# Kernel tuning notes

Hardware: AMD Instinct MI355X
Metric: run time of the kernel (lower is better)

## Reference

```python
import jax, jax.numpy as jnp
import numpy as np

N_PAPER = 200000
N_MESH = 30000
N = N_PAPER + N_MESH
D_PAPER = 512
D_MESH = 128
E_TRAIN = 2000000
E_POS = 500000
E_NEG = 500000


def setup_inputs() -> dict:
    key = jax.random.key(0)
    ks = jax.random.split(key, 32)

    def w(k, shape, fan_in):
        return jax.random.normal(k, shape, jnp.float32) / np.float32(np.sqrt(fan_in))

    inp = {}
    inp['x_paper'] = jax.random.normal(ks[0], (N_PAPER, D_PAPER), jnp.float32)
    inp['x_mesh'] = jax.random.normal(ks[1], (N_MESH, D_MESH), jnp.float32)
    # input transforms (stored as [in, out]; y = x @ W + b)
    inp['tp_w'] = w(ks[2], (D_PAPER, 16), D_PAPER)
    inp['tp_b'] = jnp.zeros((16,), jnp.float32)
    inp['tm_w'] = w(ks[3], (D_MESH, 16), D_MESH)
    inp['tm_b'] = jnp.zeros((16,), jnp.float32)
    # RGCN layers: basis decomposition W_r = sum_b comp[r,b] * basis[b]
    inp['comp1'] = w(ks[4], (2, 4), 4)
    inp['basis1'] = w(ks[5], (4, 16, 32), 16)
    inp['root1'] = w(ks[6], (16, 32), 16)
    inp['bias1'] = jnp.zeros((32,), jnp.float32)
    inp['comp2'] = w(ks[7], (2, 4), 4)
    inp['basis2'] = w(ks[8], (4, 32, 32), 32)
    inp['root2'] = w(ks[9], (32, 32), 32)
    inp['bias2'] = jnp.zeros((32,), jnp.float32)
    inp['comp3'] = w(ks[10], (2, 4), 4)
    inp['basis3'] = w(ks[11], (4, 32, 16), 32)
    inp['root3'] = w(ks[12], (32, 16), 32)
    inp['bias3'] = jnp.zeros((16,), jnp.float32)
    # decode linears (16 -> 16)
    inp['dpp_w'] = w(ks[13], (16, 16), 16)
    inp['dpp_b'] = jnp.zeros((16,), jnp.float32)
    inp['dpm_w'] = w(ks[14], (16, 16), 16)
    inp['dpm_b'] = jnp.zeros((16,), jnp.float32)
    # graph structure
    inp['train_edge_index'] = jax.random.randint(ks[15], (2, E_TRAIN), 0, N, jnp.int64)
    inp['train_edge_type'] = jax.random.randint(ks[16], (E_TRAIN,), 0, 2, jnp.int64)
    inp['pos_edge_index'] = jax.random.randint(ks[17], (2, E_POS), 0, N, jnp.int64)
    inp['pos_edge_type'] = jnp.sort(jax.random.randint(ks[18], (E_POS,), 0, 2, jnp.int64))
    inp['neg_edge_index'] = jax.random.randint(ks[19], (2, E_NEG), 0, N, jnp.int64)
    inp['neg_edge_type'] = jnp.sort(jax.random.randint(ks[20], (E_NEG,), 0, 2, jnp.int64))
    return inp


def rgcn(x, src, dst, etype, comp, basis, root, bias):
    # W: [R, in, out] from basis decomposition
    W = jnp.einsum('rb,bio->rio', comp, basis)
    # relation-typed message per edge (R == 2: compute both, select)
    xs = x[src]                                   # [E, in]  gather
    m = jnp.where((etype == 0)[:, None], xs @ W[0], xs @ W[1])  # [E, out]
    n = x.shape[0]
    agg = jax.ops.segment_sum(m, dst, num_segments=n)           # scatter-add
    deg = jax.ops.segment_sum(jnp.ones((src.shape[0],), x.dtype), dst, num_segments=n)
    agg = agg / jnp.maximum(deg, 1.0)[:, None]                   # mean aggregation
    return agg + x @ root + bias


def reference(x_paper, x_mesh, tp_w, tp_b, tm_w, tm_b,
              comp1, basis1, root1, bias1,
              comp2, basis2, root2, bias2,
              comp3, basis3, root3, bias3,
              dpp_w, dpp_b, dpm_w, dpm_b,
              train_edge_index, train_edge_type,
              pos_edge_index, pos_edge_type,
              neg_edge_index, neg_edge_type):
    # encode
    x = jnp.concatenate([x_paper @ tp_w + tp_b, x_mesh @ tm_w + tm_b], axis=0)
    src, dst = train_edge_index[0], train_edge_index[1]
    x = jax.nn.relu(rgcn(x, src, dst, train_edge_type, comp1, basis1, root1, bias1))
    x = jax.nn.relu(rgcn(x, src, dst, train_edge_type, comp2, basis2, root2, bias2))
    z = rgcn(x, src, dst, train_edge_type, comp3, basis3, root3, bias3)

    # decode: edge types are sorted, so per-edge type-select equals the
    # original mask-then-concat ordering [type0 ..., type1 ...]
    def edge_scores(ei, et):
        zs, zd = z[ei[0]], z[ei[1]]
        p = jnp.where((et == 0)[:, None], zs @ dpp_w + dpp_b, zs @ dpm_w + dpm_b)
        return (p * zd).sum(-1)

    return jnp.concatenate([edge_scores(pos_edge_index, pos_edge_type),
                            edge_scores(neg_edge_index, neg_edge_type)], axis=0)
```

## Files before the change

### kernel.cpp

```cpp
#include <hip/hip_runtime.h>

#define NPAPER 200000
#define NMESH  30000
#define NNODES 230000
#define ETRAIN 2000000
#define EPOS   500000
#define ENEG   500000

typedef _Float16 f16;
typedef __attribute__((ext_vector_type(8))) _Float16 f16x8;
typedef __attribute__((ext_vector_type(4))) _Float16 f16x4;

__device__ __forceinline__ void fma4(float4& a, float s, const float4 w) {
    a.x = fmaf(s, w.x, a.x);
    a.y = fmaf(s, w.y, a.y);
    a.z = fmaf(s, w.z, a.z);
    a.w = fmaf(s, w.w, a.w);
}

template <int D>
__global__ __launch_bounds__(256) void encode_kernel(
    const float* __restrict__ x, const float* __restrict__ w,
    const float* __restrict__ bias, float* __restrict__ out, int nrows) {
    constexpr int KP = 16;
    __shared__ float wlds[D * 16];
    __shared__ float xlds[256 * 20];
    __shared__ float blds[16];

    for (int i = threadIdx.x; i < D * 4; i += 256)
        reinterpret_cast<float4*>(wlds)[i] =
            reinterpret_cast<const float4*>(w)[i];
    if (threadIdx.x < 16) blds[threadIdx.x] = bias[threadIdx.x];

    const int g = threadIdx.x & 3;
    const int rg = threadIdx.x >> 2;
    const int row0 = blockIdx.x * 256;

    float4 acc[4];
#pragma unroll
    for (int j = 0; j < 4; j++) acc[j] = make_float4(0.f, 0.f, 0.f, 0.f);

    for (int p = 0; p < D / KP; p++) {
        __syncthreads();
        for (int i = threadIdx.x; i < 1024; i += 256) {
            const int rr = i >> 2, q = i & 3;
            const int grow = min(row0 + rr, nrows - 1);
            *reinterpret_cast<float4*>(xlds + rr * 20 + q * 4) =
                *reinterpret_cast<const float4*>(x + (size_t)grow * D +
                                                 p * KP + q * 4);
        }
        __syncthreads();
#pragma unroll
        for (int q = 0; q < KP / 4; q++) {
            const int k = p * KP + q * 4;
            const float4 w0 =
                *reinterpret_cast<const float4*>(wlds + (k + 0) * 16 + 4 * g);
            const float4 w1 =
                *reinterpret_cast<const float4*>(wlds + (k + 1) * 16 + 4 * g);
            const float4 w2 =
                *reinterpret_cast<const float4*>(wlds + (k + 2) * 16 + 4 * g);
            const float4 w3 =
                *reinterpret_cast<const float4*>(wlds + (k + 3) * 16 + 4 * g);
#pragma unroll
            for (int j = 0; j < 4; j++) {
                const float4 xv = *reinterpret_cast<const float4*>(
                    xlds + (rg + 64 * j) * 20 + q * 4);
                fma4(acc[j], xv.x, w0);
                fma4(acc[j], xv.y, w1);
                fma4(acc[j], xv.z, w2);
                fma4(acc[j], xv.w, w3);
            }
        }
    }

    const float4 b4 = *reinterpret_cast<const float4*>(blds + 4 * g);
#pragma unroll
    for (int j = 0; j < 4; j++) {
        const int grow = row0 + rg + 64 * j;
        if (grow < nrows) {
            float4 o;
            o.x = acc[j].x + b4.x;
            o.y = acc[j].y + b4.y;
            o.z = acc[j].z + b4.z;
            o.w = acc[j].w + b4.w;
            *reinterpret_cast<float4*>(out + (size_t)grow * 16 + 4 * g) = o;
        }
    }
}

__global__ __launch_bounds__(256) void hist_kernel(const int* __restrict__ dst,
                                                   int* __restrict__ cnt) {
    const int e = blockIdx.x * 256 + threadIdx.x;
    if (e >= ETRAIN) return;
    atomicAdd(cnt + dst[e], 1);
}

__global__ __launch_bounds__(256) void scan1_kernel(const int* __restrict__ in,
                                                    int* __restrict__ out,
                                                    int* __restrict__ bsum,
                                                    int n) {
    __shared__ int s[256];
    const int tid = threadIdx.x;
    const int i = blockIdx.x * 256 + tid;
    const int v = (i < n) ? in[i] : 0;
    s[tid] = v;
    __syncthreads();
#pragma unroll
    for (int off = 1; off < 256; off <<= 1) {
        const int t = (tid >= off) ? s[tid - off] : 0;
        __syncthreads();
        s[tid] += t;
        __syncthreads();
    }
    if (i < n) out[i] = s[tid] - v;
    if (tid == 255) bsum[blockIdx.x] = s[255];
}

__global__ __launch_bounds__(256) void scan2_kernel(int* __restrict__ bsum,
                                                    int nb) {
    __shared__ int s[256];
    const int tid = threadIdx.x;
    int carry = 0;
    for (int base = 0; base < nb; base += 256) {
        const int i = base + tid;
        const int v = (i < nb) ? bsum[i] : 0;
        s[tid] = v;
        __syncthreads();
#pragma unroll
        for (int off = 1; off < 256; off <<= 1) {
            const int t = (tid >= off) ? s[tid - off] : 0;
            __syncthreads();
            s[tid] += t;
            __syncthreads();
        }
        if (i < nb) bsum[i] = s[tid] - v + carry;
        const int tot = s[255];
        __syncthreads();
        carry += tot;
    }
}

__global__ __launch_bounds__(256) void fill_kernel(
    const int* __restrict__ src, const int* __restrict__ dst,
    const int* __restrict__ et, const int* __restrict__ rowptr,
    const int* __restrict__ bsum, int* __restrict__ fc,
    int* __restrict__ esorted) {
    const int e = blockIdx.x * 256 + threadIdx.x;
    if (e >= ETRAIN) return;
    const int d = dst[e];
    const int pos = rowptr[d] + bsum[d >> 8] + atomicAdd(fc + d, 1);
    esorted[pos] = src[e] | (et[e] << 24);
}

template <int IN, int OUT, bool INH>
__global__ __launch_bounds__(256) void transform_kernel(
    const void* __restrict__ xinp, const float* __restrict__ comp,
    const float* __restrict__ basis, const float* __restrict__ root,
    const float* __restrict__ bias, f16* __restrict__ tcat,
    float* __restrict__ rbuf) {
    constexpr int QP = OUT / 4;
    __shared__ float wl[3 * IN * OUT];
    __shared__ float bl[OUT];
    for (int i = threadIdx.x; i < 2 * IN * OUT; i += 256) {
        const int rr = i / (IN * OUT);
        const int rem = i - rr * IN * OUT;
        float v = 0.f;
#pragma unroll
        for (int bb = 0; bb < 4; bb++)
            v = fmaf(comp[rr * 4 + bb], basis[bb * IN * OUT + rem], v);
        wl[i] = v;
    }
    for (int i = threadIdx.x; i < IN * OUT; i += 256)
        wl[2 * IN * OUT + i] = root[i];
    if (threadIdx.x < OUT) bl[threadIdx.x] = bias[threadIdx.x];
    __syncthreads();

    const int gtid = blockIdx.x * 256 + threadIdx.x;
    const int n = gtid / QP;
    const int g = gtid % QP;
    if (n >= NNODES) return;

    float4 a0 = make_float4(0.f, 0.f, 0.f, 0.f);
    float4 a1 = a0;
    float4 ar = *reinterpret_cast<const float4*>(bl + 4 * g);

    if constexpr (INH) {
        const f16* xin = (const f16*)xinp + (size_t)n * IN;
#pragma unroll
        for (int q = 0; q < IN / 8; q++) {
            const f16x8 raw = reinterpret_cast<const f16x8*>(xin)[q];
#pragma unroll
            for (int j = 0; j < 8; j++) {
                const float xv = (float)raw[j];
                const float* w0 = wl + (q * 8 + j) * OUT + 4 * g;
                fma4(a0, xv, *reinterpret_cast<const float4*>(w0));
                fma4(a1, xv, *reinterpret_cast<const float4*>(w0 + IN * OUT));
                fma4(ar, xv,
                     *reinterpret_cast<const float4*>(w0 + 2 * IN * OUT));
            }
        }
    } else {
        const float* xin = (const float*)xinp + (size_t)n * IN;
#pragma unroll
        for (int q = 0; q < IN / 4; q++) {
            const float4 xv4 = reinterpret_cast<const float4*>(xin)[q];
            const float xs[4] = {xv4.x, xv4.y, xv4.z, xv4.w};
#pragma unroll
            for (int j = 0; j < 4; j++) {
                const float* w0 = wl + (q * 4 + j) * OUT + 4 * g;
                fma4(a0, xs[j], *reinterpret_cast<const float4*>(w0));
                fma4(a1, xs[j],
                     *reinterpret_cast<const float4*>(w0 + IN * OUT));
                fma4(ar, xs[j],
                     *reinterpret_cast<const float4*>(w0 + 2 * IN * OUT));
            }
        }
    }
    f16x4 t0, t1;
    t0[0] = (f16)a0.x; t0[1] = (f16)a0.y; t0[2] = (f16)a0.z; t0[3] = (f16)a0.w;
    t1[0] = (f16)a1.x; t1[1] = (f16)a1.y; t1[2] = (f16)a1.z; t1[3] = (f16)a1.w;
    f16* trow = tcat + (size_t)n * 2 * OUT;
    reinterpret_cast<f16x4*>(trow)[g] = t0;
    reinterpret_cast<f16x4*>(trow + OUT)[g] = t1;
    reinterpret_cast<float4*>(rbuf + (size_t)n * OUT)[g] = ar;
}

template <int OUT, bool RELU, bool OUTH>
__global__ __launch_bounds__(256) void aggroot_kernel(
    const f16* __restrict__ tcat, const float* __restrict__ rbuf,
    const int* __restrict__ rowptr, const int* __restrict__ bsum,
    const int* __restrict__ cnt, const int* __restrict__ esorted,
    void* __restrict__ outp) {
    constexpr int NF = OUT / 4;
    const int gtid = blockIdx.x * 256 + threadIdx.x;
    const int n = gtid >> 5;
    if (n >= NNODES) return;
    const int lane = gtid & 31;
    const int f = lane & 3;
    const int e = lane >> 2;
    const int b = rowptr[n] + bsum[n >> 8];
    const int c = cnt[n];

    float a[NF];
#pragma unroll
    for (int j = 0; j < NF; j++) a[j] = 0.f;

    int i = e;
    int pk = (i < c) ? esorted[b + i] : 0;
    while (i < c) {
        const int in2 = i + 8;
        const int pkn = (in2 < c) ? esorted[b + in2] : 0;
        const int s = pk & 0x00FFFFFF;
        const int t = pk >> 24;
        const f16* row = tcat + ((size_t)s * 2 + t) * OUT + f * NF;
        if constexpr (NF == 8) {
            const f16x8 raw = *reinterpret_cast<const f16x8*>(row);
#pragma unroll
            for (int j = 0; j < 8; j++) a[j] += (float)raw[j];
        } else {
            const f16x4 raw = *reinterpret_cast<const f16x4*>(row);
#pragma unroll
            for (int j = 0; j < 4; j++) a[j] += (float)raw[j];
        }
        pk = pkn;
        i = in2;
    }
#pragma unroll
    for (int m = 4; m <= 16; m <<= 1) {
#pragma unroll
        for (int j = 0; j < NF; j++) a[j] += __shfl_xor(a[j], m);
    }
    const float inv = 1.0f / fmaxf((float)c, 1.0f);
    if constexpr (NF == 8) {
        if (e < 2) {
            const int off = f * 8 + e * 4;
            const float4 rv =
                *reinterpret_cast<const float4*>(rbuf + (size_t)n * OUT + off);
            float4 v;
            v.x = fmaf(a[e * 4 + 0], inv, rv.x);
            v.y = fmaf(a[e * 4 + 1], inv, rv.y);
            v.z = fmaf(a[e * 4 + 2], inv, rv.z);
            v.w = fmaf(a[e * 4 + 3], inv, rv.w);
            if (RELU) {
                v.x = fmaxf(v.x, 0.f);
                v.y = fmaxf(v.y, 0.f);
                v.z = fmaxf(v.z, 0.f);
                v.w = fmaxf(v.w, 0.f);
            }
            if constexpr (OUTH) {
                f16x4 hv;
                hv[0] = (f16)v.x; hv[1] = (f16)v.y;
                hv[2] = (f16)v.z; hv[3] = (f16)v.w;
                *reinterpret_cast<f16x4*>((f16*)outp + (size_t)n * OUT + off) =
                    hv;
            } else {
                *reinterpret_cast<float4*>((float*)outp + (size_t)n * OUT +
                                           off) = v;
            }
        }
    } else {
        if (e == 0) {
            const int off = f * 4;
            const float4 rv =
                *reinterpret_cast<const float4*>(rbuf + (size_t)n * OUT + off);
            float4 v;
            v.x = fmaf(a[0], inv, rv.x);
            v.y = fmaf(a[1], inv, rv.y);
            v.z = fmaf(a[2], inv, rv.z);
            v.w = fmaf(a[3], inv, rv.w);
            if (RELU) {
                v.x = fmaxf(v.x, 0.f);
                v.y = fmaxf(v.y, 0.f);
                v.z = fmaxf(v.z, 0.f);
                v.w = fmaxf(v.w, 0.f);
            }
            if constexpr (OUTH) {
                f16x4 hv;
                hv[0] = (f16)v.x; hv[1] = (f16)v.y;
                hv[2] = (f16)v.z; hv[3] = (f16)v.w;
                *reinterpret_cast<f16x4*>((f16*)outp + (size_t)n * OUT + off) =
                    hv;
            } else {
                *reinterpret_cast<float4*>((float*)outp + (size_t)n * OUT +
                                           off) = v;
            }
        }
    }
}

__global__ __launch_bounds__(256) void decode_kernel(
    const float* __restrict__ z, const int* __restrict__ pei,
    const int* __restrict__ pet, const int* __restrict__ nei,
    const int* __restrict__ net, const float* __restrict__ wp,
    const float* __restrict__ bp, const float* __restrict__ wm,
    const float* __restrict__ bm, float* __restrict__ out) {
    __shared__ float wl[2 * 256];
    __shared__ float bl[2 * 16];
    {
        const int i = threadIdx.x;
        wl[i] = wp[i];
        wl[256 + i] = wm[i];
        if (i < 16) {
            bl[i] = bp[i];
            bl[16 + i] = bm[i];
        }
    }
    __syncthreads();

    const int gtid = blockIdx.x * 256 + threadIdx.x;
    const int e = gtid >> 2;
    const int f = gtid & 3;
    if (e >= EPOS + ENEG) return;
    int s, d, t;
    if (e < EPOS) {
        s = pei[e];
        d = pei[e + EPOS];
        t = pet[e];
    } else {
        const int ee = e - EPOS;
        s = nei[ee];
        d = nei[ee + ENEG];
        t = net[ee];
    }

    const float4 zs = reinterpret_cast<const float4*>(z + (size_t)s * 16)[f];
    const float4 zd = reinterpret_cast<const float4*>(z + (size_t)d * 16)[f];

    const float* W = wl + t * 256;
    float4 p[4];
    if (f == 0) {
#pragma unroll
        for (int g = 0; g < 4; g++)
            p[g] = reinterpret_cast<const float4*>(bl + t * 16)[g];
    } else {
#pragma unroll
        for (int g = 0; g < 4; g++) p[g] = make_float4(0.f, 0.f, 0.f, 0.f);
    }
    const float xs[4] = {zs.x, zs.y, zs.z, zs.w};
#pragma unroll
    for (int c = 0; c < 4; c++) {
        const float4* wr =
            reinterpret_cast<const float4*>(W + (4 * f + c) * 16);
#pragma unroll
        for (int g = 0; g < 4; g++) fma4(p[g], xs[c], wr[g]);
    }
    float* pp = reinterpret_cast<float*>(p);
#pragma unroll
    for (int m = 1; m <= 2; m <<= 1) {
#pragma unroll
        for (int j = 0; j < 16; j++) pp[j] += __shfl_xor(pp[j], m);
    }
    float4 pf;
    if (f == 0) pf = p[0];
    else if (f == 1) pf = p[1];
    else if (f == 2) pf = p[2];
    else pf = p[3];
    float sc = pf.x * zd.x + pf.y * zd.y + pf.z * zd.z + pf.w * zd.w;
    sc += __shfl_xor(sc, 1);
    sc += __shfl_xor(sc, 2);
    if (f == 0) out[e] = sc;
}

extern "C" void kernel_launch(void* const* d_in, const int* in_sizes, int n_in,
                              void* d_out, int out_size, void* d_ws,
                              size_t ws_size, hipStream_t stream) {
    const float* x_paper = (const float*)d_in[0];
    const float* x_mesh = (const float*)d_in[1];
    const float* tp_w = (const float*)d_in[2];
    const float* tp_b = (const float*)d_in[3];
    const float* tm_w = (const float*)d_in[4];
    const float* tm_b = (const float*)d_in[5];
    const float* comp1 = (const float*)d_in[6];
    const float* basis1 = (const float*)d_in[7];
    const float* root1 = (const float*)d_in[8];
    const float* bias1 = (const float*)d_in[9];
    const float* comp2 = (const float*)d_in[10];
    const float* basis2 = (const float*)d_in[11];
    const float* root2 = (const float*)d_in[12];
    const float* bias2 = (const float*)d_in[13];
    const float* comp3 = (const float*)d_in[14];
    const float* basis3 = (const float*)d_in[15];
    const float* root3 = (const float*)d_in[16];
    const float* bias3 = (const float*)d_in[17];
    const float* dpp_w = (const float*)d_in[18];
    const float* dpp_b = (const float*)d_in[19];
    const float* dpm_w = (const float*)d_in[20];
    const float* dpm_b = (const float*)d_in[21];
    const int* tei = (const int*)d_in[22];
    const int* tet = (const int*)d_in[23];
    const int* pei = (const int*)d_in[24];
    const int* pet = (const int*)d_in[25];
    const int* nei = (const int*)d_in[26];
    const int* net = (const int*)d_in[27];
    float* out = (float*)d_out;

    const size_t N = NNODES;
    float* ws = (float*)d_ws;
    float* xfeat = ws;
    float* z = ws + 16 * N;
    float* rbuf = ws + 32 * N;
    f16* tcat = (f16*)(ws + 64 * N);
    f16* h1 = (f16*)(ws + 96 * N);
    f16* h2 = (f16*)(ws + 112 * N);
    int* rowptr = (int*)(ws + 128 * N);
    int* ecnt = rowptr + N;
    int* fc = ecnt + N;
    int* esorted = fc + N;
    int* bsum = esorted + ETRAIN;

    const int* tsrc = tei;
    const int* tdst = tei + ETRAIN;

    const int eblocks = (ETRAIN + 255) / 256;
    const int nb = (NNODES + 255) / 256;
    const int aggb = (NNODES * 32 + 255) / 256;

    encode_kernel<512><<<(NPAPER + 255) / 256, 256, 0, stream>>>(
        x_paper, tp_w, tp_b, xfeat, NPAPER);
    encode_kernel<128><<<(NMESH + 255) / 256, 256, 0, stream>>>(
        x_mesh, tm_w, tm_b, xfeat + (size_t)NPAPER * 16, NMESH);

    hipMemsetAsync(ecnt, 0, (size_t)2 * NNODES * 4, stream);
    hist_kernel<<<eblocks, 256, 0, stream>>>(tdst, ecnt);
    scan1_kernel<<<nb, 256, 0, stream>>>(ecnt, rowptr, bsum, NNODES);
    scan2_kernel<<<1, 256, 0, stream>>>(bsum, nb);
    fill_kernel<<<eblocks, 256, 0, stream>>>(tsrc, tdst, tet, rowptr, bsum,
                                             fc, esorted);

    transform_kernel<16, 32, false>
        <<<(NNODES * 8 + 255) / 256, 256, 0, stream>>>(xfeat, comp1, basis1,
                                                       root1, bias1, tcat,
                                                       rbuf);
    aggroot_kernel<32, true, true><<<aggb, 256, 0, stream>>>(
        tcat, rbuf, rowptr, bsum, ecnt, esorted, h1);

    transform_kernel<32, 32, true>
        <<<(NNODES * 8 + 255) / 256, 256, 0, stream>>>(h1, comp2, basis2,
                                                       root2, bias2, tcat,
                                                       rbuf);
    aggroot_kernel<32, true, true><<<aggb, 256, 0, stream>>>(
        tcat, rbuf, rowptr, bsum, ecnt, esorted, h2);

    transform_kernel<32, 16, true>
        <<<(NNODES * 4 + 255) / 256, 256, 0, stream>>>(h2, comp3, basis3,
                                                       root3, bias3, tcat,
                                                       rbuf);
    aggroot_kernel<16, false, false><<<aggb, 256, 0, stream>>>(
        tcat, rbuf, rowptr, bsum, ecnt, esorted, z);

    decode_kernel<<<((EPOS + ENEG) * 4 + 255) / 256, 256, 0, stream>>>(
        z, pei, pet, nei, net, dpp_w, dpp_b, dpm_w, dpm_b, out);
}
```

Measured before the change: 1.152 ms.

## Precompute per-node decode projections and store root/z buffers in fp16

Decoding now projects every node through both decode linears once (uproj_kernel) instead of recomputing the 16x16 projection per edge, so each edge does only a 16-wide dot product against precomputed fp16 rows. The root-transform buffer and the final embedding z are stored in fp16, halving their memory traffic. Per-node projection adds work over 230k nodes for both types while removing per-edge matmuls on 1M edges, and the extra fp16 rounding adds precision risk.

```diff
diff --git a/kernel.cpp b/kernel.cpp
--- a/kernel.cpp
+++ b/kernel.cpp
@@ -157,7 +157,7 @@
     const void* __restrict__ xinp, const float* __restrict__ comp,
     const float* __restrict__ basis, const float* __restrict__ root,
     const float* __restrict__ bias, f16* __restrict__ tcat,
-    float* __restrict__ rbuf) {
+    f16* __restrict__ rbuf) {
     constexpr int QP = OUT / 4;
     __shared__ float wl[3 * IN * OUT];
     __shared__ float bl[OUT];
@@ -216,18 +216,19 @@
             }
         }
     }
-    f16x4 t0, t1;
+    f16x4 t0, t1, tr;
     t0[0] = (f16)a0.x; t0[1] = (f16)a0.y; t0[2] = (f16)a0.z; t0[3] = (f16)a0.w;
     t1[0] = (f16)a1.x; t1[1] = (f16)a1.y; t1[2] = (f16)a1.z; t1[3] = (f16)a1.w;
+    tr[0] = (f16)ar.x; tr[1] = (f16)ar.y; tr[2] = (f16)ar.z; tr[3] = (f16)ar.w;
     f16* trow = tcat + (size_t)n * 2 * OUT;
     reinterpret_cast<f16x4*>(trow)[g] = t0;
     reinterpret_cast<f16x4*>(trow + OUT)[g] = t1;
-    reinterpret_cast<float4*>(rbuf + (size_t)n * OUT)[g] = ar;
+    reinterpret_cast<f16x4*>(rbuf + (size_t)n * OUT)[g] = tr;
 }
 
 template <int OUT, bool RELU, bool OUTH>
 __global__ __launch_bounds__(256) void aggroot_kernel(
-    const f16* __restrict__ tcat, const float* __restrict__ rbuf,
+    const f16* __restrict__ tcat, const f16* __restrict__ rbuf,
     const int* __restrict__ rowptr, const int* __restrict__ bsum,
     const int* __restrict__ cnt, const int* __restrict__ esorted,
     void* __restrict__ outp) {
@@ -274,13 +275,13 @@
     if constexpr (NF == 8) {
         if (e < 2) {
             const int off = f * 8 + e * 4;
-            const float4 rv =
-                *reinterpret_cast<const float4*>(rbuf + (size_t)n * OUT + off);
+            const f16x4 rv =
+                *reinterpret_cast<const f16x4*>(rbuf + (size_t)n * OUT + off);
             float4 v;
-            v.x = fmaf(a[e * 4 + 0], inv, rv.x);
-            v.y = fmaf(a[e * 4 + 1], inv, rv.y);
-            v.z = fmaf(a[e * 4 + 2], inv, rv.z);
-            v.w = fmaf(a[e * 4 + 3], inv, rv.w);
+            v.x = fmaf(a[e * 4 + 0], inv, (float)rv[0]);
+            v.y = fmaf(a[e * 4 + 1], inv, (float)rv[1]);
+            v.z = fmaf(a[e * 4 + 2], inv, (float)rv[2]);
+            v.w = fmaf(a[e * 4 + 3], inv, (float)rv[3]);
             if (RELU) {
                 v.x = fmaxf(v.x, 0.f);
                 v.y = fmaxf(v.y, 0.f);
@@ -301,13 +302,13 @@
     } else {
         if (e == 0) {
             const int off = f * 4;
-            const float4 rv =
-                *reinterpret_cast<const float4*>(rbuf + (size_t)n * OUT + off);
+            const f16x4 rv =
+                *reinterpret_cast<const f16x4*>(rbuf + (size_t)n * OUT + off);
             float4 v;
-            v.x = fmaf(a[0], inv, rv.x);
-            v.y = fmaf(a[1], inv, rv.y);
-            v.z = fmaf(a[2], inv, rv.z);
-            v.w = fmaf(a[3], inv, rv.w);
+            v.x = fmaf(a[0], inv, (float)rv[0]);
+            v.y = fmaf(a[1], inv, (float)rv[1]);
+            v.z = fmaf(a[2], inv, (float)rv[2]);
+            v.w = fmaf(a[3], inv, (float)rv[3]);
             if (RELU) {
                 v.x = fmaxf(v.x, 0.f);
                 v.y = fmaxf(v.y, 0.f);
@@ -328,12 +329,10 @@
     }
 }
 
-__global__ __launch_bounds__(256) void decode_kernel(
-    const float* __restrict__ z, const int* __restrict__ pei,
-    const int* __restrict__ pet, const int* __restrict__ nei,
-    const int* __restrict__ net, const float* __restrict__ wp,
+__global__ __launch_bounds__(256) void uproj_kernel(
+    const f16* __restrict__ zh, const float* __restrict__ wp,
     const float* __restrict__ bp, const float* __restrict__ wm,
-    const float* __restrict__ bm, float* __restrict__ out) {
+    const float* __restrict__ bm, f16* __restrict__ u) {
     __shared__ float wl[2 * 256];
     __shared__ float bl[2 * 16];
     {
@@ -346,10 +345,48 @@
         }
     }
     __syncthreads();
-
     const int gtid = blockIdx.x * 256 + threadIdx.x;
-    const int e = gtid >> 2;
-    const int f = gtid & 3;
+    const int n = gtid >> 1;
+    const int t = gtid & 1;
+    if (n >= NNODES) return;
+    const f16x8 z0 = reinterpret_cast<const f16x8*>(zh + (size_t)n * 16)[0];
+    const f16x8 z1 = reinterpret_cast<const f16x8*>(zh + (size_t)n * 16)[1];
+    float acc[16];
+#pragma unroll
+    for (int j = 0; j < 16; j++) acc[j] = bl[t * 16 + j];
+    const float* W = wl + t * 256;
+#pragma unroll
+    for (int k = 0; k < 8; k++) {
+        const float zk = (float)z0[k];
+#pragma unroll
+        for (int j = 0; j < 16; j++) acc[j] = fmaf(zk, W[k * 16 + j], acc[j]);
+    }
+#pragma unroll
+    for (int k = 0; k < 8; k++) {
+        const float zk = (float)z1[k];
+#pragma unroll
+        for (int j = 0; j < 16; j++)
+            acc[j] = fmaf(zk, W[(8 + k) * 16 + j], acc[j]);
+    }
+    f16x8 o0, o1;
+#pragma unroll
+    for (int j = 0; j < 8; j++) {
+        o0[j] = (f16)acc[j];
+        o1[j] = (f16)acc[8 + j];
+    }
+    f16* ur = u + (size_t)n * 32 + t * 16;
+    reinterpret_cast<f16x8*>(ur)[0] = o0;
+    reinterpret_cast<f16x8*>(ur)[1] = o1;
+}
+
+__global__ __launch_bounds__(256) void decode_kernel(
+    const f16* __restrict__ u, const f16* __restrict__ zh,
+    const int* __restrict__ pei, const int* __restrict__ pet,
+    const int* __restrict__ nei, const int* __restrict__ net,
+    float* __restrict__ out) {
+    const int gtid = blockIdx.x * 256 + threadIdx.x;
+    const int e = gtid >> 1;
+    const int h = gtid & 1;
     if (e >= EPOS + ENEG) return;
     int s, d, t;
     if (e < EPOS) {
@@ -362,43 +399,15 @@
         d = nei[ee + ENEG];
         t = net[ee];
     }
-
-    const float4 zs = reinterpret_cast<const float4*>(z + (size_t)s * 16)[f];
-    const float4 zd = reinterpret_cast<const float4*>(z + (size_t)d * 16)[f];
-
-    const float* W = wl + t * 256;
-    float4 p[4];
-    if (f == 0) {
-#pragma unroll
-        for (int g = 0; g < 4; g++)
-            p[g] = reinterpret_cast<const float4*>(bl + t * 16)[g];
-    } else {
-#pragma unroll
-        for (int g = 0; g < 4; g++) p[g] = make_float4(0.f, 0.f, 0.f, 0.f);
-    }
-    const float xs[4] = {zs.x, zs.y, zs.z, zs.w};
-#pragma unroll
-    for (int c = 0; c < 4; c++) {
-        const float4* wr =
-            reinterpret_cast<const float4*>(W + (4 * f + c) * 16);
-#pragma unroll
-        for (int g = 0; g < 4; g++) fma4(p[g], xs[c], wr[g]);
-    }
-    float* pp = reinterpret_cast<float*>(p);
-#pragma unroll
-    for (int m = 1; m <= 2; m <<= 1) {
-#pragma unroll
-        for (int j = 0; j < 16; j++) pp[j] += __shfl_xor(pp[j], m);
-    }
-    float4 pf;
-    if (f == 0) pf = p[0];
-    else if (f == 1) pf = p[1];
-    else if (f == 2) pf = p[2];
-    else pf = p[3];
-    float sc = pf.x * zd.x + pf.y * zd.y + pf.z * zd.z + pf.w * zd.w;
+    const f16x8 uv =
+        *reinterpret_cast<const f16x8*>(u + (size_t)s * 32 + t * 16 + h * 8);
+    const f16x8 zv =
+        *reinterpret_cast<const f16x8*>(zh + (size_t)d * 16 + h * 8);
+    float sc = 0.f;
+#pragma unroll
+    for (int j = 0; j < 8; j++) sc = fmaf((float)uv[j], (float)zv[j], sc);
     sc += __shfl_xor(sc, 1);
-    sc += __shfl_xor(sc, 2);
-    if (f == 0) out[e] = sc;
+    if (h == 0) out[e] = sc;
 }
 
 extern "C" void kernel_launch(void* const* d_in, const int* in_sizes, int n_in,
@@ -437,12 +446,13 @@
     const size_t N = NNODES;
     float* ws = (float*)d_ws;
     float* xfeat = ws;
-    float* z = ws + 16 * N;
-    float* rbuf = ws + 32 * N;
-    f16* tcat = (f16*)(ws + 64 * N);
-    f16* h1 = (f16*)(ws + 96 * N);
-    f16* h2 = (f16*)(ws + 112 * N);
-    int* rowptr = (int*)(ws + 128 * N);
+    f16* rbuf = (f16*)(ws + 16 * N);
+    f16* tcat = (f16*)(ws + 32 * N);
+    f16* h1 = (f16*)(ws + 64 * N);
+    f16* h2 = (f16*)(ws + 80 * N);
+    f16* zh = (f16*)(ws + 96 * N);
+    f16* u = (f16*)(ws + 104 * N);
+    int* rowptr = (int*)(ws + 120 * N);
     int* ecnt = rowptr + N;
     int* fc = ecnt + N;
     int* esorted = fc + N;
@@ -485,9 +495,11 @@
         <<<(NNODES * 4 + 255) / 256, 256, 0, stream>>>(h2, comp3, basis3,
                                                        root3, bias3, tcat,
                                                        rbuf);
-    aggroot_kernel<16, false, false><<<aggb, 256, 0, stream>>>(
-        tcat, rbuf, rowptr, bsum, ecnt, esorted, z);
-
-    decode_kernel<<<((EPOS + ENEG) * 4 + 255) / 256, 256, 0, stream>>>(
-        z, pei, pet, nei, net, dpp_w, dpp_b, dpm_w, dpm_b, out);
-}
+    aggroot_kernel<16, false, true><<<aggb, 256, 0, stream>>>(
+        tcat, rbuf, rowptr, bsum, ecnt, esorted, zh);
+
+    uproj_kernel<<<(NNODES * 2 + 255) / 256, 256, 0, stream>>>(
+        zh, dpp_w, dpp_b, dpm_w, dpm_b, u);
+    decode_kernel<<<((EPOS + ENEG) * 2 + 255) / 256, 256, 0, stream>>>(
+        u, zh, pei, pet, nei, net, out);
+}
```

Result: no change. 1.144 ms (-0.7%).
